# Optimization experiments

Measured on AMD Instinct MI355X. Metric: run time of the kernel, lower is better.

The kernel has to match this reference:

```python
import jax, jax.numpy as jnp
import numpy as np

HEADS = 4
HID = 256
MAX_OFFSET = 2


def setup_inputs() -> dict:
    key = jax.random.key(0)
    ks = jax.random.split(key, 8)
    B, T, C = 4, 512, HID
    x = jax.random.normal(ks[0], (B, T, C), jnp.float32)
    mask = jax.random.randint(ks[1], (B, 1, T), 0, 2).astype(bool)
    s2 = 1.0 / np.sqrt(2 * C)
    s1 = 1.0 / np.sqrt(C)
    W_subj = jax.random.uniform(ks[2], (2 * C, C), jnp.float32, -s2, s2)
    b_subj = jax.random.uniform(ks[3], (C,), jnp.float32, -s2, s2)
    W_obj = jax.random.uniform(ks[4], (2 * C, C), jnp.float32, -s2, s2)
    b_obj = jax.random.uniform(ks[5], (C,), jnp.float32, -s2, s2)
    W_t = jax.random.uniform(ks[6], (C, HEADS), jnp.float32, -s1, s1)
    b_t = jax.random.uniform(ks[7], (HEADS,), jnp.float32, -s1, s1)
    return {"x": x, "W_subj": W_subj, "b_subj": b_subj, "W_obj": W_obj,
            "b_obj": b_obj, "W_t": W_t, "b_t": b_t, "mask": mask}


def reference(x, W_subj, b_subj, W_obj, b_obj, W_t, b_t, mask):
    # x: [B,T,C]. torch MaxPool1d on [B,T,C] pools over the LAST dim (C),
    # kernel = 2*MAX_OFFSET+1, stride 1, same padding (pad value -inf).
    k = 2 * MAX_OFFSET + 1
    x_pooled = jax.lax.reduce_window(
        x, -jnp.inf, jax.lax.max,
        window_dimensions=(1, 1, k), window_strides=(1, 1, 1),
        padding=[(0, 0), (0, 0), (MAX_OFFSET, MAX_OFFSET)])
    x_new = jnp.concatenate([x_pooled, x], axis=2)      # [B,T,2C]
    subj = x_new @ W_subj + b_subj                      # [B,T,C]
    obj = x_new @ W_obj + b_obj                         # [B,T,C]
    # subj.unsqueeze(1): varies over axis 2; obj.unsqueeze(2): varies over axis 1
    abs_multi = jnp.abs(subj[:, None, :, :] - obj[:, :, None, :])  # [B,T,T,C]
    rep = abs_multi @ W_t + b_t                         # [B,T,T,H]
    attn = jax.nn.softmax(jax.nn.relu(rep), axis=2)     # softmax over obj axis
    m = mask[:, 0, :]                                   # [B,T]
    mm = m[:, None, :] & m[:, :, None]                  # [B,T,T]
    attn = jnp.where(mm[..., None], 0.0, attn)          # masked_fill -> 0
    return x_new, attn  # attn[..., h] == attn_adj_list[h]
```

## Files before the change

### kernel.cpp

```cpp
#include <hip/hip_runtime.h>
#include <hip/hip_bf16.h>
#include <math.h>

#define NB 4
#define NT 512
#define NC 256
#define NC2 512
#define NH 4

typedef __attribute__((ext_vector_type(8))) short bf16x8;
typedef __attribute__((ext_vector_type(4))) float f32x4;

__device__ inline unsigned short f2bf(float f) {
    unsigned u = __float_as_uint(f);
    unsigned r = (u + 0x7fffu + ((u >> 16) & 1u)) >> 16;
    return (unsigned short)r;
}

__global__ void k_mask(const unsigned char* __restrict__ raw, int* __restrict__ out) {
    __shared__ int s_bytes;
    if (threadIdx.x == 0) s_bytes = 0;
    __syncthreads();
    int flag = 0;
    const unsigned* w = (const unsigned*)raw;
    for (int i = threadIdx.x; i < (NB * NT) / 4; i += blockDim.x)
        if (w[i] > 1u) flag = 1;
    if (flag) atomicOr(&s_bytes, 1);
    __syncthreads();
    const int ib = s_bytes;
    for (int i = threadIdx.x; i < NB * NT; i += blockDim.x) {
        int v = ib ? (int)raw[i] : ((const int*)raw)[i];
        out[i] = v ? 1 : 0;
    }
}

__global__ void k_pool(const float* __restrict__ x, float* __restrict__ xnew,
                       unsigned short* __restrict__ xb) {
    const int row = blockIdx.x;
    const int c = threadIdx.x;
    __shared__ float r[NC];
    r[c] = x[(size_t)row * NC + c];
    __syncthreads();
    float m = r[c];
    if (c >= 1) m = fmaxf(m, r[c - 1]);
    if (c >= 2) m = fmaxf(m, r[c - 2]);
    if (c <= 254) m = fmaxf(m, r[c + 1]);
    if (c <= 253) m = fmaxf(m, r[c + 2]);
    float* o = xnew + (size_t)row * NC2;
    o[c] = m;
    o[NC + c] = r[c];
    unsigned short* ob = xb + (size_t)row * NC2;
    ob[c] = f2bf(m);
    ob[NC + c] = f2bf(r[c]);
}

__global__ void k_wcast(const float* __restrict__ Ws, const float* __restrict__ Wo,
                        unsigned short* __restrict__ wbt) {
    __shared__ float lds[32][33];
    const int kb = blockIdx.x >> 4;
    const int nb = blockIdx.x & 15;
    const int tx = threadIdx.x & 31;
    const int ty8 = threadIdx.x >> 5;
    const int n0 = nb * 32;
    const int k0 = kb * 32;
    const float* src = (n0 < 256) ? Ws : Wo;
    const int ncol = n0 & 255;
#pragma unroll
    for (int rr = 0; rr < 4; ++rr) {
        int kl = ty8 * 4 + rr;
        lds[kl][tx] = src[(size_t)(k0 + kl) * NC + ncol + tx];
    }
    __syncthreads();
#pragma unroll
    for (int rr = 0; rr < 4; ++rr) {
        int nl = ty8 * 4 + rr;
        wbt[(size_t)(n0 + nl) * NC2 + k0 + tx] = f2bf(lds[tx][nl]);
    }
}

#define MFMA_B16(A, B, C) __builtin_amdgcn_mfma_f32_16x16x32_bf16(A, B, C, 0, 0, 0)
__global__ __launch_bounds__(256) void k_gemm(
    const unsigned short* __restrict__ xb, const unsigned short* __restrict__ wbt,
    const float* __restrict__ bs, const float* __restrict__ bo,
    float* __restrict__ subj, float* __restrict__ obj) {
    const int bx = blockIdx.x;
    const int m0 = (bx >> 3) * 64;
    const int n0 = (bx & 7) * 64;
    const int w = threadIdx.x >> 6, lane = threadIdx.x & 63;
    const int wm = m0 + (w >> 1) * 32;
    const int wn = n0 + (w & 1) * 32;
    const int r = lane & 15, kg = lane >> 4;

    const unsigned short* aB0 = xb + (size_t)(wm + r) * NC2 + kg * 8;
    const unsigned short* aB1 = aB0 + 16 * NC2;
    const unsigned short* bB0 = wbt + (size_t)(wn + r) * NC2 + kg * 8;
    const unsigned short* bB1 = bB0 + 16 * NC2;

    f32x4 acc00 = {0.f, 0.f, 0.f, 0.f}, acc01 = {0.f, 0.f, 0.f, 0.f};
    f32x4 acc10 = {0.f, 0.f, 0.f, 0.f}, acc11 = {0.f, 0.f, 0.f, 0.f};

    bf16x8 a0 = *(const bf16x8*)(aB0);
    bf16x8 a1 = *(const bf16x8*)(aB1);
    bf16x8 b0 = *(const bf16x8*)(bB0);
    bf16x8 b1 = *(const bf16x8*)(bB1);

    for (int kk = 0; kk < NC2; kk += 64) {
        bf16x8 a0n = *(const bf16x8*)(aB0 + kk + 32);
        bf16x8 a1n = *(const bf16x8*)(aB1 + kk + 32);
        bf16x8 b0n = *(const bf16x8*)(bB0 + kk + 32);
        bf16x8 b1n = *(const bf16x8*)(bB1 + kk + 32);
        acc00 = MFMA_B16(a0, b0, acc00);
        acc01 = MFMA_B16(a0, b1, acc01);
        acc10 = MFMA_B16(a1, b0, acc10);
        acc11 = MFMA_B16(a1, b1, acc11);
        if (kk + 64 < NC2) {
            a0 = *(const bf16x8*)(aB0 + kk + 64);
            a1 = *(const bf16x8*)(aB1 + kk + 64);
            b0 = *(const bf16x8*)(bB0 + kk + 64);
            b1 = *(const bf16x8*)(bB1 + kk + 64);
        }
        acc00 = MFMA_B16(a0n, b0n, acc00);
        acc01 = MFMA_B16(a0n, b1n, acc01);
        acc10 = MFMA_B16(a1n, b0n, acc10);
        acc11 = MFMA_B16(a1n, b1n, acc11);
    }

#define EPI(ACC, S, T) { \
    const int col = wn + (T) * 16 + r; \
    const int rowb = wm + (S) * 16 + kg * 4; \
    const float bias = (col < NC) ? bs[col] : bo[col - NC]; \
    float* outp = (col < NC) ? (subj + col) : (obj + col - NC); \
    _Pragma("unroll") \
    for (int e = 0; e < 4; ++e) outp[(size_t)(rowb + e) * NC] = ACC[e] + bias; }
    EPI(acc00, 0, 0) EPI(acc01, 0, 1) EPI(acc10, 1, 0) EPI(acc11, 1, 1)
#undef EPI
}

#define OF32(r) ((r) * 36 + (((r) >> 2) << 2))
__global__ __launch_bounds__(256) void k_rep(
    const float* __restrict__ subj, const float* __restrict__ obj,
    const float* __restrict__ Wt, const float* __restrict__ bt,
    float* __restrict__ attn) {
    const int bx = blockIdx.x;
    const int b = bx >> 8;
    const int rem = bx & 255;
    const int it = rem >> 4, jt = rem & 15;
    const int i0 = it * 32, j0 = jt * 32;
    const int bNT = b * NT;

    __shared__ float sjT[2368];
    __shared__ float obT[2368];
    __shared__ float wt4[NC * 4];

    const int tid = threadIdx.x;
    const int tx = tid & 15;
    const int ty = tid >> 4;
    const int ja = tid >> 4;
    const int c4a = tid & 15;

    {
        float4 wv = ((const float4*)Wt)[tid];
        *(float4*)&wt4[tid * 4] = wv;
    }

    float acc[2][2][4];
#pragma unroll
    for (int ii = 0; ii < 2; ++ii)
#pragma unroll
        for (int jj = 0; jj < 2; ++jj)
#pragma unroll
            for (int h = 0; h < 4; ++h) acc[ii][jj][h] = 0.f;

    float4 vs0, vs1, vo0, vo1;
#define LOADCH(CC) { \
    vs0 = *(const float4*)(subj + ((size_t)(bNT + j0 + ja)) * NC + (CC) + c4a * 4); \
    vs1 = *(const float4*)(subj + ((size_t)(bNT + j0 + ja + 16)) * NC + (CC) + c4a * 4); \
    vo0 = *(const float4*)(obj  + ((size_t)(bNT + i0 + ja)) * NC + (CC) + c4a * 4); \
    vo1 = *(const float4*)(obj  + ((size_t)(bNT + i0 + ja + 16)) * NC + (CC) + c4a * 4); }

    LOADCH(0)

    for (int cc = 0; cc < NC; cc += 64) {
        if (cc) __syncthreads();
        {
            const int rb = c4a * 4;
            sjT[OF32(rb + 0) + ja] = vs0.x; sjT[OF32(rb + 1) + ja] = vs0.y;
            sjT[OF32(rb + 2) + ja] = vs0.z; sjT[OF32(rb + 3) + ja] = vs0.w;
            sjT[OF32(rb + 0) + ja + 16] = vs1.x; sjT[OF32(rb + 1) + ja + 16] = vs1.y;
            sjT[OF32(rb + 2) + ja + 16] = vs1.z; sjT[OF32(rb + 3) + ja + 16] = vs1.w;
            obT[OF32(rb + 0) + ja] = vo0.x; obT[OF32(rb + 1) + ja] = vo0.y;
            obT[OF32(rb + 2) + ja] = vo0.z; obT[OF32(rb + 3) + ja] = vo0.w;
            obT[OF32(rb + 0) + ja + 16] = vo1.x; obT[OF32(rb + 1) + ja + 16] = vo1.y;
            obT[OF32(rb + 2) + ja + 16] = vo1.z; obT[OF32(rb + 3) + ja + 16] = vo1.w;
        }
        __syncthreads();
        if (cc + 64 < NC) LOADCH(cc + 64)

#pragma unroll 8
        for (int cl = 0; cl < 64; ++cl) {
            const float2 s2 = *(const float2*)&sjT[OF32(cl) + tx * 2];
            const float2 o2 = *(const float2*)&obT[OF32(cl) + ty * 2];
            const float4 w4 = *(const float4*)&wt4[(cc + cl) * 4];
            const float sv[2] = {s2.x, s2.y};
            const float ov[2] = {o2.x, o2.y};
#pragma unroll
            for (int ii = 0; ii < 2; ++ii)
#pragma unroll
                for (int jj = 0; jj < 2; ++jj) {
                    const float d = fabsf(sv[jj] - ov[ii]);
                    acc[ii][jj][0] = fmaf(d, w4.x, acc[ii][jj][0]);
                    acc[ii][jj][1] = fmaf(d, w4.y, acc[ii][jj][1]);
                    acc[ii][jj][2] = fmaf(d, w4.z, acc[ii][jj][2]);
                    acc[ii][jj][3] = fmaf(d, w4.w, acc[ii][jj][3]);
                }
        }
    }
#undef LOADCH

    const float4 btv = *(const float4*)bt;
#pragma unroll
    for (int ii = 0; ii < 2; ++ii) {
        const int i = i0 + ty * 2 + ii;
#pragma unroll
        for (int jj = 0; jj < 2; ++jj) {
            const int j = j0 + tx * 2 + jj;
            float4 rr;
            rr.x = fmaxf(acc[ii][jj][0] + btv.x, 0.f);
            rr.y = fmaxf(acc[ii][jj][1] + btv.y, 0.f);
            rr.z = fmaxf(acc[ii][jj][2] + btv.z, 0.f);
            rr.w = fmaxf(acc[ii][jj][3] + btv.w, 0.f);
            *(float4*)&attn[(((size_t)bNT + i) * NT + j) * NH] = rr;
        }
    }
}

__global__ __launch_bounds__(256) void k_soft(float* __restrict__ attn,
                                              const int* __restrict__ mask) {
    const int wv = threadIdx.x >> 6, lane = threadIdx.x & 63;
    const int bi = blockIdx.x * 4 + wv;
    const int b = bi >> 9;
    float4* row = (float4*)(attn + (size_t)bi * (NT * NH));

    float4 v[8];
#pragma unroll
    for (int q = 0; q < 8; ++q) v[q] = row[lane + 64 * q];

    float mx[4];
#pragma unroll
    for (int h = 0; h < 4; ++h) {
        float m = ((const float*)&v[0])[h];
#pragma unroll
        for (int q = 1; q < 8; ++q) m = fmaxf(m, ((const float*)&v[q])[h]);
        mx[h] = m;
    }
#pragma unroll
    for (int off = 32; off; off >>= 1) {
#pragma unroll
        for (int h = 0; h < 4; ++h) mx[h] = fmaxf(mx[h], __shfl_xor(mx[h], off));
    }

    float sm[4] = {0.f, 0.f, 0.f, 0.f};
#pragma unroll
    for (int q = 0; q < 8; ++q) {
        float4 e;
        e.x = expf(v[q].x - mx[0]); e.y = expf(v[q].y - mx[1]);
        e.z = expf(v[q].z - mx[2]); e.w = expf(v[q].w - mx[3]);
        v[q] = e;
        sm[0] += e.x; sm[1] += e.y; sm[2] += e.z; sm[3] += e.w;
    }
#pragma unroll
    for (int off = 32; off; off >>= 1) {
#pragma unroll
        for (int h = 0; h < 4; ++h) sm[h] += __shfl_xor(sm[h], off);
    }
    float rinv[4];
#pragma unroll
    for (int h = 0; h < 4; ++h) rinv[h] = 1.0f / sm[h];

    const int mi = mask[bi];
#pragma unroll
    for (int q = 0; q < 8; ++q) {
        const int mj = mask[b * NT + lane + 64 * q];
        const bool z = (mi & mj);
        float4 o;
        o.x = z ? 0.f : v[q].x * rinv[0];
        o.y = z ? 0.f : v[q].y * rinv[1];
        o.z = z ? 0.f : v[q].z * rinv[2];
        o.w = z ? 0.f : v[q].w * rinv[3];
        row[lane + 64 * q] = o;
    }
}

extern "C" void kernel_launch(void* const* d_in, const int* in_sizes, int n_in,
                              void* d_out, int out_size, void* d_ws, size_t ws_size,
                              hipStream_t stream) {
    const float* x      = (const float*)d_in[0];
    const float* W_subj = (const float*)d_in[1];
    const float* b_subj = (const float*)d_in[2];
    const float* W_obj  = (const float*)d_in[3];
    const float* b_obj  = (const float*)d_in[4];
    const float* W_t    = (const float*)d_in[5];
    const float* b_t    = (const float*)d_in[6];
    const unsigned char* mask_raw = (const unsigned char*)d_in[7];

    float* xnew = (float*)d_out;
    float* attn = xnew + (size_t)NB * NT * NC2;

    int* wmask          = (int*)d_ws;
    float* subj         = (float*)((char*)d_ws + 8192);
    float* obj          = subj + (size_t)NB * NT * NC;
    unsigned short* xb  = (unsigned short*)(obj + (size_t)NB * NT * NC);
    unsigned short* wbt = xb + (size_t)NB * NT * NC2;

    hipLaunchKernelGGL(k_mask, dim3(1), dim3(256), 0, stream, mask_raw, wmask);
    hipLaunchKernelGGL(k_pool, dim3(NB * NT), dim3(NC), 0, stream, x, xnew, xb);
    hipLaunchKernelGGL(k_wcast, dim3(256), dim3(256), 0, stream, W_subj, W_obj, wbt);
    hipLaunchKernelGGL(k_gemm, dim3(256), dim3(256), 0, stream,
                       xb, wbt, b_subj, b_obj, subj, obj);
    hipLaunchKernelGGL(k_rep, dim3(NB * 16 * 16), dim3(256), 0, stream,
                       subj, obj, W_t, b_t, attn);
    hipLaunchKernelGGL(k_soft, dim3(NB * NT / 4), dim3(256), 0, stream, attn, wmask);
}
```

Baseline: 140.5 us.

## Split channel reduction across waves with 4x4 tiles, packed FMA and LDS reduction

Each of the four waves in a k_rep block now handles a 16-channel slice of every 64-channel chunk for the whole 32x32 tile. Each lane computes a 4x4 (i,j) sub-tile using packed two-wide float FMAs, and the four partial sums are combined through LDS in a tree reduction before wave 0 writes the output. Wt is read straight from global memory instead of being staged in LDS, and launch bounds request 3 blocks per CU. The goal is more arithmetic per LDS load and use of packed FP32 math, paid for with more registers per lane (64 accumulators), extra synchronisation for the reduction, and only one wave doing the epilogue stores.

```diff
diff --git a/kernel.cpp b/kernel.cpp
--- a/kernel.cpp
+++ b/kernel.cpp
@@ -10,6 +10,7 @@
 
 typedef __attribute__((ext_vector_type(8))) short bf16x8;
 typedef __attribute__((ext_vector_type(4))) float f32x4;
+typedef __attribute__((ext_vector_type(2))) float f32x2;
 
 __device__ inline unsigned short f2bf(float f) {
     unsigned u = __float_as_uint(f);
@@ -137,7 +138,7 @@
 }
 
 #define OF32(r) ((r) * 36 + (((r) >> 2) << 2))
-__global__ __launch_bounds__(256) void k_rep(
+__global__ __launch_bounds__(256, 3) void k_rep(
     const float* __restrict__ subj, const float* __restrict__ obj,
     const float* __restrict__ Wt, const float* __restrict__ bt,
     float* __restrict__ attn) {
@@ -148,88 +149,153 @@
     const int i0 = it * 32, j0 = jt * 32;
     const int bNT = b * NT;
 
-    __shared__ float sjT[2368];
-    __shared__ float obT[2368];
-    __shared__ float wt4[NC * 4];
+    __shared__ float lds_buf[4736];
+    float* sjT = lds_buf;
+    float* obT = lds_buf + 2368;
 
     const int tid = threadIdx.x;
-    const int tx = tid & 15;
-    const int ty = tid >> 4;
-    const int ja = tid >> 4;
+    const int cs = __builtin_amdgcn_readfirstlane(tid >> 6);
+    const int lane = tid & 63;
+    const int tx4 = (lane & 7) * 4;
+    const int ty4 = (lane >> 3) * 4;
+    const int csB = cs * 16;
+
     const int c4a = tid & 15;
-
-    {
-        float4 wv = ((const float4*)Wt)[tid];
-        *(float4*)&wt4[tid * 4] = wv;
-    }
-
-    float acc[2][2][4];
-#pragma unroll
-    for (int ii = 0; ii < 2; ++ii)
-#pragma unroll
-        for (int jj = 0; jj < 2; ++jj)
-#pragma unroll
-            for (int h = 0; h < 4; ++h) acc[ii][jj][h] = 0.f;
+    const int jb = tid >> 4;
+
+    const float4* WtV = (const float4*)Wt;
+
+    f32x2 acc[4][2][4];
+#pragma unroll
+    for (int ii = 0; ii < 4; ++ii)
+#pragma unroll
+        for (int jp = 0; jp < 2; ++jp)
+#pragma unroll
+            for (int h = 0; h < 4; ++h) acc[ii][jp][h] = (f32x2){0.f, 0.f};
 
     float4 vs0, vs1, vo0, vo1;
 #define LOADCH(CC) { \
-    vs0 = *(const float4*)(subj + ((size_t)(bNT + j0 + ja)) * NC + (CC) + c4a * 4); \
-    vs1 = *(const float4*)(subj + ((size_t)(bNT + j0 + ja + 16)) * NC + (CC) + c4a * 4); \
-    vo0 = *(const float4*)(obj  + ((size_t)(bNT + i0 + ja)) * NC + (CC) + c4a * 4); \
-    vo1 = *(const float4*)(obj  + ((size_t)(bNT + i0 + ja + 16)) * NC + (CC) + c4a * 4); }
+    vs0 = *(const float4*)(subj + ((size_t)(bNT + j0 + jb)) * NC + (CC) + c4a * 4); \
+    vs1 = *(const float4*)(subj + ((size_t)(bNT + j0 + jb + 16)) * NC + (CC) + c4a * 4); \
+    vo0 = *(const float4*)(obj  + ((size_t)(bNT + i0 + jb)) * NC + (CC) + c4a * 4); \
+    vo1 = *(const float4*)(obj  + ((size_t)(bNT + i0 + jb + 16)) * NC + (CC) + c4a * 4); }
 
     LOADCH(0)
 
-    for (int cc = 0; cc < NC; cc += 64) {
+    for (int cc = 0; cc < 4; ++cc) {
+        const int cc64 = cc * 64;
         if (cc) __syncthreads();
         {
             const int rb = c4a * 4;
-            sjT[OF32(rb + 0) + ja] = vs0.x; sjT[OF32(rb + 1) + ja] = vs0.y;
-            sjT[OF32(rb + 2) + ja] = vs0.z; sjT[OF32(rb + 3) + ja] = vs0.w;
-            sjT[OF32(rb + 0) + ja + 16] = vs1.x; sjT[OF32(rb + 1) + ja + 16] = vs1.y;
-            sjT[OF32(rb + 2) + ja + 16] = vs1.z; sjT[OF32(rb + 3) + ja + 16] = vs1.w;
-            obT[OF32(rb + 0) + ja] = vo0.x; obT[OF32(rb + 1) + ja] = vo0.y;
-            obT[OF32(rb + 2) + ja] = vo0.z; obT[OF32(rb + 3) + ja] = vo0.w;
-            obT[OF32(rb + 0) + ja + 16] = vo1.x; obT[OF32(rb + 1) + ja + 16] = vo1.y;
-            obT[OF32(rb + 2) + ja + 16] = vo1.z; obT[OF32(rb + 3) + ja + 16] = vo1.w;
-        }
-        __syncthreads();
-        if (cc + 64 < NC) LOADCH(cc + 64)
+            sjT[OF32(rb + 0) + jb] = vs0.x; sjT[OF32(rb + 1) + jb] = vs0.y;
+            sjT[OF32(rb + 2) + jb] = vs0.z; sjT[OF32(rb + 3) + jb] = vs0.w;
+            sjT[OF32(rb + 0) + jb + 16] = vs1.x; sjT[OF32(rb + 1) + jb + 16] = vs1.y;
+            sjT[OF32(rb + 2) + jb + 16] = vs1.z; sjT[OF32(rb + 3) + jb + 16] = vs1.w;
+            obT[OF32(rb + 0) + jb] = vo0.x; obT[OF32(rb + 1) + jb] = vo0.y;
+            obT[OF32(rb + 2) + jb] = vo0.z; obT[OF32(rb + 3) + jb] = vo0.w;
+            obT[OF32(rb + 0) + jb + 16] = vo1.x; obT[OF32(rb + 1) + jb + 16] = vo1.y;
+            obT[OF32(rb + 2) + jb + 16] = vo1.z; obT[OF32(rb + 3) + jb + 16] = vo1.w;
+        }
+        __syncthreads();
+        if (cc + 1 < 4) LOADCH(cc64 + 64)
 
 #pragma unroll 8
-        for (int cl = 0; cl < 64; ++cl) {
-            const float2 s2 = *(const float2*)&sjT[OF32(cl) + tx * 2];
-            const float2 o2 = *(const float2*)&obT[OF32(cl) + ty * 2];
-            const float4 w4 = *(const float4*)&wt4[(cc + cl) * 4];
-            const float sv[2] = {s2.x, s2.y};
-            const float ov[2] = {o2.x, o2.y};
-#pragma unroll
-            for (int ii = 0; ii < 2; ++ii)
-#pragma unroll
-                for (int jj = 0; jj < 2; ++jj) {
-                    const float d = fabsf(sv[jj] - ov[ii]);
-                    acc[ii][jj][0] = fmaf(d, w4.x, acc[ii][jj][0]);
-                    acc[ii][jj][1] = fmaf(d, w4.y, acc[ii][jj][1]);
-                    acc[ii][jj][2] = fmaf(d, w4.z, acc[ii][jj][2]);
-                    acc[ii][jj][3] = fmaf(d, w4.w, acc[ii][jj][3]);
-                }
+        for (int q = 0; q < 16; ++q) {
+            const int cl = csB + q;
+            const float4 sv4 = *(const float4*)&sjT[OF32(cl) + tx4];
+            const float4 ov4 = *(const float4*)&obT[OF32(cl) + ty4];
+            const float4 w4 = WtV[cc64 + cl];
+            const f32x2 s01 = {sv4.x, sv4.y};
+            const f32x2 s23 = {sv4.z, sv4.w};
+            const f32x2 w0 = {w4.x, w4.x};
+            const f32x2 w1 = {w4.y, w4.y};
+            const f32x2 w2 = {w4.z, w4.z};
+            const f32x2 w3 = {w4.w, w4.w};
+#define IIBLK(II, OV) { \
+    const f32x2 ob2 = {OV, OV}; \
+    const f32x2 d01 = s01 - ob2; \
+    const f32x2 d23 = s23 - ob2; \
+    f32x2 a01, a23; \
+    a01.x = fabsf(d01.x); a01.y = fabsf(d01.y); \
+    a23.x = fabsf(d23.x); a23.y = fabsf(d23.y); \
+    acc[II][0][0] = a01 * w0 + acc[II][0][0]; \
+    acc[II][0][1] = a01 * w1 + acc[II][0][1]; \
+    acc[II][0][2] = a01 * w2 + acc[II][0][2]; \
+    acc[II][0][3] = a01 * w3 + acc[II][0][3]; \
+    acc[II][1][0] = a23 * w0 + acc[II][1][0]; \
+    acc[II][1][1] = a23 * w1 + acc[II][1][1]; \
+    acc[II][1][2] = a23 * w2 + acc[II][1][2]; \
+    acc[II][1][3] = a23 * w3 + acc[II][1][3]; }
+            IIBLK(0, ov4.x) IIBLK(1, ov4.y) IIBLK(2, ov4.z) IIBLK(3, ov4.w)
+#undef IIBLK
         }
     }
 #undef LOADCH
 
-    const float4 btv = *(const float4*)bt;
-#pragma unroll
-    for (int ii = 0; ii < 2; ++ii) {
-        const int i = i0 + ty * 2 + ii;
-#pragma unroll
-        for (int jj = 0; jj < 2; ++jj) {
-            const int j = j0 + tx * 2 + jj;
-            float4 rr;
-            rr.x = fmaxf(acc[ii][jj][0] + btv.x, 0.f);
-            rr.y = fmaxf(acc[ii][jj][1] + btv.y, 0.f);
-            rr.z = fmaxf(acc[ii][jj][2] + btv.z, 0.f);
-            rr.w = fmaxf(acc[ii][jj][3] + btv.w, 0.f);
-            *(float4*)&attn[(((size_t)bNT + i) * NT + j) * NH] = rr;
+    float* rbuf = lds_buf;
+    const int lb = lane * 36;
+#pragma unroll
+    for (int half = 0; half < 2; ++half) {
+        __syncthreads();
+        if (cs == 1 || cs == 3) {
+            float* p = rbuf + ((cs == 1) ? 0 : 2368) + lb;
+#pragma unroll
+            for (int k = 0; k < 16; ++k)
+                *(f32x2*)(p + k * 2) = acc[half * 2 + (k >> 3)][(k >> 2) & 1][k & 3];
+        }
+        __syncthreads();
+        if (cs == 0 || cs == 2) {
+            const float* p = rbuf + ((cs == 0) ? 0 : 2368) + lb;
+#pragma unroll
+            for (int k = 0; k < 16; ++k)
+                acc[half * 2 + (k >> 3)][(k >> 2) & 1][k & 3] += *(const f32x2*)(p + k * 2);
+        }
+    }
+#pragma unroll
+    for (int half = 0; half < 2; ++half) {
+        __syncthreads();
+        if (cs == 2) {
+            float* p = rbuf + lb;
+#pragma unroll
+            for (int k = 0; k < 16; ++k)
+                *(f32x2*)(p + k * 2) = acc[half * 2 + (k >> 3)][(k >> 2) & 1][k & 3];
+        }
+        __syncthreads();
+        if (cs == 0) {
+            const float* p = rbuf + lb;
+#pragma unroll
+            for (int k = 0; k < 16; ++k)
+                acc[half * 2 + (k >> 3)][(k >> 2) & 1][k & 3] += *(const f32x2*)(p + k * 2);
+        }
+    }
+
+    if (cs == 0) {
+        const float4 btv = *(const float4*)bt;
+#pragma unroll
+        for (int ii = 0; ii < 4; ++ii) {
+            const int i = i0 + ty4 + ii;
+            float* orow = attn + (((size_t)(bNT + i)) * NT + (j0 + tx4)) * NH;
+            float4 r0, r1, r2, r3;
+            r0.x = fmaxf(acc[ii][0][0].x + btv.x, 0.f);
+            r0.y = fmaxf(acc[ii][0][1].x + btv.y, 0.f);
+            r0.z = fmaxf(acc[ii][0][2].x + btv.z, 0.f);
+            r0.w = fmaxf(acc[ii][0][3].x + btv.w, 0.f);
+            r1.x = fmaxf(acc[ii][0][0].y + btv.x, 0.f);
+            r1.y = fmaxf(acc[ii][0][1].y + btv.y, 0.f);
+            r1.z = fmaxf(acc[ii][0][2].y + btv.z, 0.f);
+            r1.w = fmaxf(acc[ii][0][3].y + btv.w, 0.f);
+            r2.x = fmaxf(acc[ii][1][0].x + btv.x, 0.f);
+            r2.y = fmaxf(acc[ii][1][1].x + btv.y, 0.f);
+            r2.z = fmaxf(acc[ii][1][2].x + btv.z, 0.f);
+            r2.w = fmaxf(acc[ii][1][3].x + btv.w, 0.f);
+            r3.x = fmaxf(acc[ii][1][0].y + btv.x, 0.f);
+            r3.y = fmaxf(acc[ii][1][1].y + btv.y, 0.f);
+            r3.z = fmaxf(acc[ii][1][2].y + btv.z, 0.f);
+            r3.w = fmaxf(acc[ii][1][3].y + btv.w, 0.f);
+            *(float4*)(orow + 0)  = r0;
+            *(float4*)(orow + 4)  = r1;
+            *(float4*)(orow + 8)  = r2;
+            *(float4*)(orow + 12) = r3;
         }
     }
 }
```

After: 137.2 us. -2.4%, faster.
